# Optimization experiments

Hardware: AMD Instinct MI355X
Metric: run time of the kernel (lower is better)

## Reference

```python
import jax, jax.numpy as jnp
import numpy as np

DIM = 4096
N_HEADS = 32
HEAD_DIM = DIM // N_HEADS  # 128
SEQ = 2048
BATCH = 2


def _rope_freqs(seq_len, head_dim, theta=10000.0):
    inv = 1.0 / (theta ** (np.arange(0, head_dim, 2, dtype=np.float32) / head_dim))
    ang = np.outer(np.arange(seq_len, dtype=np.float32), inv)  # [S, hd/2]
    return jnp.asarray(np.cos(ang)), jnp.asarray(np.sin(ang))


def setup_inputs() -> dict:
    key = jax.random.key(0)
    ks = jax.random.split(key, 10)
    s = 1.0 / np.sqrt(DIM)
    inp = {
        "x": jax.random.normal(ks[0], (BATCH, SEQ, DIM), dtype=jnp.float32),
        "wq_w": jax.random.normal(ks[1], (DIM, DIM), dtype=jnp.float32) * s,
        "wq_b": jax.random.normal(ks[2], (DIM,), dtype=jnp.float32) * 0.01,
        "wk_w": jax.random.normal(ks[3], (DIM, DIM), dtype=jnp.float32) * s,
        "wk_b": jax.random.normal(ks[4], (DIM,), dtype=jnp.float32) * 0.01,
        "wv_w": jax.random.normal(ks[5], (DIM, DIM), dtype=jnp.float32) * s,
        "wv_b": jax.random.normal(ks[6], (DIM,), dtype=jnp.float32) * 0.01,
        "wo_w": jax.random.normal(ks[7], (DIM, DIM), dtype=jnp.float32) * s,
        "wo_b": jax.random.normal(ks[8], (DIM,), dtype=jnp.float32) * 0.01,
    }
    cos, sin = _rope_freqs(SEQ, HEAD_DIM)
    inp["freqs_cos"] = cos  # [S, hd/2]
    inp["freqs_sin"] = sin
    return inp


def _apply_rope(x, cos, sin):
    # x: [B, S, H, D]; cos/sin: [S, D/2] -> broadcast [1, S, 1, D/2]
    B, S, H, D = x.shape
    xr = x.reshape(B, S, H, D // 2, 2)
    re, im = xr[..., 0], xr[..., 1]
    c = cos[None, :, None, :]
    s = sin[None, :, None, :]
    out_re = re * c - im * s
    out_im = re * s + im * c
    return jnp.stack([out_re, out_im], axis=-1).reshape(B, S, H, D)


def reference(x, freqs_cos, freqs_sin, wq_w, wq_b, wk_w, wk_b, wv_w, wv_b, wo_w, wo_b):
    B, S, C = x.shape
    H, D = N_HEADS, HEAD_DIM
    xq = (x @ wq_w.T + wq_b).reshape(B, S, H, D)
    xk = (x @ wk_w.T + wk_b).reshape(B, S, H, D)
    xv = (x @ wv_w.T + wv_b).reshape(B, S, H, D)
    xq = _apply_rope(xq, freqs_cos, freqs_sin)
    xk = _apply_rope(xk, freqs_cos, freqs_sin)
    # [B, H, S, D]
    xq = xq.transpose(0, 2, 1, 3)
    xk = xk.transpose(0, 2, 1, 3)
    xv = xv.transpose(0, 2, 1, 3)
    scale = 1.0 / jnp.sqrt(jnp.asarray(D, dtype=x.dtype))
    scores = jnp.einsum('bhsd,bhtd->bhst', xq, xk) * scale
    causal = jnp.tril(jnp.ones((S, S), dtype=bool))
    scores = jnp.where(causal[None, None], scores, jnp.asarray(-jnp.inf, dtype=scores.dtype))
    attn = jax.nn.softmax(scores, axis=-1)
    y = jnp.einsum('bhst,bhtd->bhsd', attn, xv)  # [B, H, S, D]
    # faithful to source: transpose(-1,-2) then view(B, S, -1) -> raw reshape of [B,H,D,S]
    y = y.transpose(0, 1, 3, 2).reshape(B, S, H * D)
    return y @ wo_w.T + wo_b
```

## Files before the change

### kernel.cpp

```cpp
#include <hip/hip_runtime.h>
#include <hip/hip_bf16.h>

typedef __hip_bfloat16 bf16;
typedef short s16x8 __attribute__((ext_vector_type(8)));
typedef float fx4 __attribute__((ext_vector_type(4)));
typedef unsigned int u32;

#define DIM 4096
#define SEQ 2048
#define NH 32
#define HD 128

#define MFMA_BF16(a,b,c) __builtin_amdgcn_mfma_f32_16x16x32_bf16((a),(b),(c),0,0,0)

__device__ __forceinline__ void gload16(const bf16* g, const bf16* l) {
  __builtin_amdgcn_global_load_lds((const __attribute__((address_space(1))) u32*)g,
                                   (__attribute__((address_space(3))) u32*)l, 16, 0, 0);
}

__global__ void cvt_f32_bf16(const float* __restrict__ in, bf16* __restrict__ out, int n8)
{
  int i = blockIdx.x * blockDim.x + threadIdx.x;
  const int stride = gridDim.x * blockDim.x;
  for (; i < n8; i += stride) {
    fx4 a = ((const fx4*)in)[2 * i], b = ((const fx4*)in)[2 * i + 1];
    s16x8 o; bf16* op = (bf16*)&o;
    #pragma unroll
    for (int j = 0; j < 4; ++j) { op[j] = __float2bfloat16(a[j]); op[4 + j] = __float2bfloat16(b[j]); }
    ((s16x8*)out)[i] = o;
  }
}

__global__ __launch_bounds__(512, 1)
void gemm256(const bf16* __restrict__ A, const bf16* __restrict__ W,
             const float* __restrict__ bias,
             const float* __restrict__ fcos, const float* __restrict__ fsin,
             void* __restrict__ outv, int mode)
{
  __shared__ __align__(16) bf16 As[2][256 * 64];
  __shared__ __align__(16) bf16 Bs[2][256 * 64];
  const int tid = threadIdx.x;
  const int wid = tid >> 6;
  const int lane = tid & 63;
  const int l15 = lane & 15, lg = lane >> 4;
  const int wm = wid >> 2, wn = wid & 3;
  const int brow = blockIdx.y * 256, bcol = blockIdx.x * 256;
  const int rsub = lane >> 3;
  const int scol = ((lane & 7) ^ rsub) * 8;

  fx4 acc[8][4] = {};

  #pragma unroll
  for (int tt = 0; tt < 2; ++tt) {
    #pragma unroll
    for (int j = 0; j < 4; ++j) {
      const int chunk = j * 8 + wid;
      const int row = chunk * 8 + rsub;
      gload16(A + (size_t)(brow + row) * DIM + tt * 64 + scol, &As[tt][chunk * 512]);
      gload16(W + (size_t)(bcol + row) * DIM + tt * 64 + scol, &Bs[tt][chunk * 512]);
    }
  }

  for (int t = 0; t < 64; ++t) {
    const int p = t & 1;
    if (t < 63) asm volatile("s_waitcnt vmcnt(8)" ::: "memory");
    else        asm volatile("s_waitcnt vmcnt(0)" ::: "memory");
    __builtin_amdgcn_s_barrier();
    __builtin_amdgcn_sched_barrier(0);

    s16x8 afr[2][8], bfr[2][4];
    #pragma unroll
    for (int kk = 0; kk < 2; ++kk) {
      #pragma unroll
      for (int mi = 0; mi < 8; ++mi) {
        const int r = wm * 128 + mi * 16 + l15;
        afr[kk][mi] = *(const s16x8*)&As[p][r * 64 + ((((kk * 4 + lg)) ^ (r & 7)) << 3)];
      }
      #pragma unroll
      for (int nj = 0; nj < 4; ++nj) {
        const int r = wn * 64 + nj * 16 + l15;
        bfr[kk][nj] = *(const s16x8*)&Bs[p][r * 64 + ((((kk * 4 + lg)) ^ (r & 7)) << 3)];
      }
    }
    asm volatile("s_waitcnt lgkmcnt(0)" ::: "memory");
    __builtin_amdgcn_sched_barrier(0);
    __builtin_amdgcn_s_barrier();
    __builtin_amdgcn_sched_barrier(0);

    if (t + 2 < 64) {
      const int k0 = (t + 2) * 64;
      #pragma unroll
      for (int j = 0; j < 4; ++j) {
        const int chunk = j * 8 + wid;
        const int row = chunk * 8 + rsub;
        gload16(A + (size_t)(brow + row) * DIM + k0 + scol, &As[p][chunk * 512]);
        gload16(W + (size_t)(bcol + row) * DIM + k0 + scol, &Bs[p][chunk * 512]);
      }
    }

    __builtin_amdgcn_s_setprio(1);
    #pragma unroll
    for (int kk = 0; kk < 2; ++kk)
      #pragma unroll
      for (int mi = 0; mi < 8; ++mi)
        #pragma unroll
        for (int nj = 0; nj < 4; ++nj)
          acc[mi][nj] = MFMA_BF16(afr[kk][mi], bfr[kk][nj], acc[mi][nj]);
    __builtin_amdgcn_s_setprio(0);
  }

  #pragma unroll
  for (int mi = 0; mi < 8; ++mi) {
    const int mbase = brow + wm * 128 + mi * 16 + lg * 4;
    #pragma unroll
    for (int nj = 0; nj < 4; ++nj) {
      const int n = bcol + wn * 64 + nj * 16 + l15;
      const float bv = bias[n];
      #pragma unroll
      for (int r = 0; r < 4; ++r) {
        const int m = mbase + r;
        float val = acc[mi][nj][r] + bv;
        if (mode <= 1) {
          const float pv = __shfl_xor(val, 1);
          const int sp = m & (SEQ - 1);
          const int fi = (n >> 1) & 63;
          const float c = fcos[sp * 64 + fi];
          const float s = fsin[sp * 64 + fi];
          val = (n & 1) ? (pv * s + val * c) : (val * c - pv * s);
        }
        if (mode == 3) {
          ((float*)outv)[(size_t)m * DIM + n] = val;
        } else {
          const int b = m >> 11, sp = m & (SEQ - 1);
          const int h = n >> 7, d = n & (HD - 1);
          ((bf16*)outv)[((size_t)(b * NH + h) * SEQ + sp) * HD + d] = __float2bfloat16(val);
        }
      }
    }
  }
}

__global__ __launch_bounds__(256, 2)
void gemm_slow(const void* __restrict__ Av, const float* __restrict__ Wf,
               const float* __restrict__ bias,
               const float* __restrict__ fcos, const float* __restrict__ fsin,
               void* __restrict__ outv, int mode)
{
  __shared__ __align__(16) bf16 As[128 * 64];
  __shared__ __align__(16) bf16 Bs[128 * 64];
  const int abf = (mode == 3) ? 1 : 0;
  const int tid = threadIdx.x;
  const int wid = tid >> 6;
  const int lane = tid & 63;
  const int l15 = lane & 15, lg = lane >> 4;
  const int wr = wid >> 1, wc = wid & 1;
  const int brow = blockIdx.y * 128, bcol = blockIdx.x * 128;

  fx4 acc[4][4] = {};

  for (int k0 = 0; k0 < DIM; k0 += 64) {
    #pragma unroll
    for (int i = 0; i < 4; ++i) {
      const int v = i * 256 + tid;
      const int row = v >> 3;
      const int c8 = (v & 7) * 8;
      s16x8 a, b;
      if (abf) {
        a = *(const s16x8*)&((const bf16*)Av)[(size_t)(brow + row) * DIM + k0 + c8];
      } else {
        const float* Af = (const float*)Av;
        fx4 a0 = *(const fx4*)&Af[(size_t)(brow + row) * DIM + k0 + c8];
        fx4 a1 = *(const fx4*)&Af[(size_t)(brow + row) * DIM + k0 + c8 + 4];
        bf16* ap = (bf16*)&a;
        #pragma unroll
        for (int j = 0; j < 4; ++j) { ap[j] = __float2bfloat16(a0[j]); ap[4 + j] = __float2bfloat16(a1[j]); }
      }
      {
        fx4 b0 = *(const fx4*)&Wf[(size_t)(bcol + row) * DIM + k0 + c8];
        fx4 b1 = *(const fx4*)&Wf[(size_t)(bcol + row) * DIM + k0 + c8 + 4];
        bf16* bp = (bf16*)&b;
        #pragma unroll
        for (int j = 0; j < 4; ++j) { bp[j] = __float2bfloat16(b0[j]); bp[4 + j] = __float2bfloat16(b1[j]); }
      }
      *(s16x8*)&As[row * 64 + c8] = a;
      *(s16x8*)&Bs[row * 64 + c8] = b;
    }
    __syncthreads();
    #pragma unroll
    for (int kk = 0; kk < 2; ++kk) {
      s16x8 af[4], bfr[4];
      #pragma unroll
      for (int mi = 0; mi < 4; ++mi)
        af[mi] = *(const s16x8*)&As[(wr * 64 + mi * 16 + l15) * 64 + kk * 32 + lg * 8];
      #pragma unroll
      for (int nj = 0; nj < 4; ++nj)
        bfr[nj] = *(const s16x8*)&Bs[(wc * 64 + nj * 16 + l15) * 64 + kk * 32 + lg * 8];
      #pragma unroll
      for (int mi = 0; mi < 4; ++mi)
        #pragma unroll
        for (int nj = 0; nj < 4; ++nj)
          acc[mi][nj] = MFMA_BF16(af[mi], bfr[nj], acc[mi][nj]);
    }
    __syncthreads();
  }

  #pragma unroll
  for (int mi = 0; mi < 4; ++mi) {
    const int mbase = brow + wr * 64 + mi * 16 + lg * 4;
    #pragma unroll
    for (int nj = 0; nj < 4; ++nj) {
      const int n = bcol + wc * 64 + nj * 16 + l15;
      const float bv = bias[n];
      #pragma unroll
      for (int r = 0; r < 4; ++r) {
        const int m = mbase + r;
        float val = acc[mi][nj][r] + bv;
        if (mode <= 1) {
          const float pv = __shfl_xor(val, 1);
          const int sp = m & (SEQ - 1);
          const int fi = (n >> 1) & 63;
          const float c = fcos[sp * 64 + fi];
          const float s = fsin[sp * 64 + fi];
          val = (n & 1) ? (pv * s + val * c) : (val * c - pv * s);
        }
        if (mode == 3) {
          ((float*)outv)[(size_t)m * DIM + n] = val;
        } else {
          const int b = m >> 11, sp = m & (SEQ - 1);
          const int h = n >> 7, d = n & (HD - 1);
          ((bf16*)outv)[((size_t)(b * NH + h) * SEQ + sp) * HD + d] = __float2bfloat16(val);
        }
      }
    }
  }
}

#define SOFTMAX_PHASE(sa, o, mrun, lrun, q0)                                   \
  {                                                                            \
    _Pragma("unroll")                                                          \
    for (int r = 0; r < 4; ++r) {                                              \
      const int q = (q0) + lg * 4 + r;                                         \
      float mx = -__builtin_inff();                                            \
      _Pragma("unroll")                                                        \
      for (int nj = 0; nj < 4; ++nj) {                                         \
        float v = sa[nj][r] * scale;                                           \
        if (diagM && (t0 + nj * 16 + l15 > q)) v = -__builtin_inff();          \
        sa[nj][r] = v;                                                         \
        mx = fmaxf(mx, v);                                                     \
      }                                                                        \
      _Pragma("unroll")                                                        \
      for (int off = 1; off < 16; off <<= 1) mx = fmaxf(mx, __shfl_xor(mx, off)); \
      const float mnew = fmaxf(mrun[r], mx);                                   \
      const float fsc = __expf(mrun[r] - mnew);                                \
      mrun[r] = mnew;                                                          \
      float rs = 0.f;                                                          \
      _Pragma("unroll")                                                        \
      for (int nj = 0; nj < 4; ++nj) {                                         \
        const float pp = __expf(sa[nj][r] - mnew);                             \
        sa[nj][r] = pp;                                                        \
        rs += pp;                                                              \
      }                                                                        \
      _Pragma("unroll")                                                        \
      for (int off = 1; off < 16; off <<= 1) rs += __shfl_xor(rs, off);        \
      lrun[r] = lrun[r] * fsc + rs;                                            \
      _Pragma("unroll")                                                        \
      for (int dj = 0; dj < 8; ++dj) o[dj][r] *= fsc;                          \
    }                                                                          \
  }

__global__ __launch_bounds__(256, 2)
void attn_fwd(const bf16* __restrict__ Q, const bf16* __restrict__ K,
              const bf16* __restrict__ V, bf16* __restrict__ ymat)
{
  __shared__ __align__(16) bf16 smem[32768];
  bf16* Kl   = smem;
  bf16* Vrow = smem + 8192;
  bf16* Vt   = smem + 16384;
  bf16* PlA  = smem + 24576;
  bf16* PlB  = smem + 28672;
  bf16* Ys   = smem;

  const int tid = threadIdx.x, wid = tid >> 6, lane = tid & 63;
  const int l15 = lane & 15, lg = lane >> 4;
  const int pair = blockIdx.x, bh = blockIdx.y;
  const int qtA = pair, qtB = 31 - pair;
  const int b = bh >> 5, h = bh & 31;
  const bf16* Qb = Q + (size_t)bh * SEQ * HD;
  const bf16* Kb = K + (size_t)bh * SEQ * HD;
  const bf16* Vb = V + (size_t)bh * SEQ * HD;
  const int q0A = qtA * 64 + wid * 16;
  const int q0B = qtB * 64 + wid * 16;

  s16x8 aqA[4], aqB[4];
  #pragma unroll
  for (int kk = 0; kk < 4; ++kk) {
    aqA[kk] = *(const s16x8*)&Qb[(size_t)(q0A + l15) * HD + kk * 32 + lg * 8];
    aqB[kk] = *(const s16x8*)&Qb[(size_t)(q0B + l15) * HD + kk * 32 + lg * 8];
  }

  fx4 oA[8] = {}, oB[8] = {};
  float mA[4], lA[4], mB[4], lB[4];
  #pragma unroll
  for (int r = 0; r < 4; ++r) {
    mA[r] = -__builtin_inff(); lA[r] = 0.f;
    mB[r] = -__builtin_inff(); lB[r] = 0.f;
  }
  const float scale = 0.08838834764831845f;

  s16x8 kreg[4], vreg[4];
  #pragma unroll
  for (int i = 0; i < 4; ++i) {
    const int chunk = i * 4 + wid;
    const int row = chunk * 4 + lg;
    const int col = ((l15 ^ (row & 7)) * 8);
    kreg[i] = *(const s16x8*)&Kb[(size_t)row * HD + col];
    vreg[i] = *(const s16x8*)&Vb[(size_t)row * HD + col];
  }

  for (int kt = 0; kt <= qtB; ++kt) {
    const int t0 = kt * 64;
    const bool doA = (kt <= qtA);

    #pragma unroll
    for (int i = 0; i < 4; ++i) {
      const int chunk = i * 4 + wid;
      *(s16x8*)((char*)Kl + chunk * 1024 + lane * 16) = kreg[i];
      *(s16x8*)((char*)Vrow + chunk * 1024 + lane * 16) = vreg[i];
    }
    __syncthreads();

    if (kt < qtB) {
      const int t1 = t0 + 64;
      #pragma unroll
      for (int i = 0; i < 4; ++i) {
        const int chunk = i * 4 + wid;
        const int row = chunk * 4 + lg;
        const int col = ((l15 ^ (row & 7)) * 8);
        kreg[i] = *(const s16x8*)&Kb[(size_t)(t1 + row) * HD + col];
        vreg[i] = *(const s16x8*)&Vb[(size_t)(t1 + row) * HD + col];
      }
    }

    fx4 sA[4], sB[4];
    #pragma unroll
    for (int nj = 0; nj < 4; ++nj) {
      fx4 sa = {}, sb = {};
      #pragma unroll
      for (int kk = 0; kk < 4; ++kk) {
        const int trow = nj * 16 + l15;
        const int colp = (kk * 32 + lg * 8) ^ ((trow & 7) << 3);
        s16x8 bk = *(const s16x8*)&Kl[trow * HD + colp];
        sb = MFMA_BF16(aqB[kk], bk, sb);
        if (doA) sa = MFMA_BF16(aqA[kk], bk, sa);
      }
      sB[nj] = sb; sA[nj] = sa;
    }

    #pragma unroll
    for (int it = 0; it < 2; ++it) {
      const int p = lane;
      const int tg = it * 4 + wid;
      s16x8 lo, hi; bf16* lop = (bf16*)&lo; bf16* hip = (bf16*)&hi;
      #pragma unroll
      for (int j = 0; j < 8; ++j) {
        const int t = tg * 8 + j;
        const u32 v32 = *(const u32*)((const char*)Vrow + t * 256 + ((p * 4) ^ (j << 4)));
        lop[j] = ((const bf16*)&v32)[0];
        hip[j] = ((const bf16*)&v32)[1];
      }
      *(s16x8*)((char*)Vt + (2 * p) * 128 + ((tg * 16) ^ ((p & 7) << 4))) = lo;
      *(s16x8*)((char*)Vt + (2 * p + 1) * 128 + ((tg * 16) ^ ((p & 7) << 4))) = hi;
    }

    {
      const bool diagM = (kt == qtB);
      SOFTMAX_PHASE(sB, oB, mB, lB, q0B)
      #pragma unroll
      for (int r = 0; r < 4; ++r) {
        const int row = lg * 4 + r;
        #pragma unroll
        for (int nj = 0; nj < 4; ++nj) {
          const int colp = (nj * 16 + l15) ^ ((row & 7) << 3);
          PlB[wid * 1024 + row * 64 + colp] = __float2bfloat16(sB[nj][r]);
        }
      }
    }
    if (doA) {
      const bool diagM = (kt == qtA);
      SOFTMAX_PHASE(sA, oA, mA, lA, q0A)
      #pragma unroll
      for (int r = 0; r < 4; ++r) {
        const int row = lg * 4 + r;
        #pragma unroll
        for (int nj = 0; nj < 4; ++nj) {
          const int colp = (nj * 16 + l15) ^ ((row & 7) << 3);
          PlA[wid * 1024 + row * 64 + colp] = __float2bfloat16(sA[nj][r]);
        }
      }
    }
    __syncthreads();

    s16x8 paA[2], paB[2];
    #pragma unroll
    for (int k2 = 0; k2 < 2; ++k2) {
      const int colp = (k2 * 32 + lg * 8) ^ ((l15 & 7) << 3);
      paB[k2] = *(const s16x8*)&PlB[wid * 1024 + l15 * 64 + colp];
      if (doA) paA[k2] = *(const s16x8*)&PlA[wid * 1024 + l15 * 64 + colp];
    }
    #pragma unroll
    for (int dj = 0; dj < 8; ++dj) {
      const int d = dj * 16 + l15;
      #pragma unroll
      for (int k2 = 0; k2 < 2; ++k2) {
        const int colp = (k2 * 32 + lg * 8) ^ (((d >> 1) & 7) << 3);
        s16x8 bv = *(const s16x8*)&Vt[d * 64 + colp];
        oB[dj] = MFMA_BF16(paB[k2], bv, oB[dj]);
        if (doA) oA[dj] = MFMA_BF16(paA[k2], bv, oA[dj]);
      }
    }
    __syncthreads();
  }

  #pragma unroll
  for (int dj = 0; dj < 8; ++dj) {
    const int d = dj * 16 + l15;
    const int lr = d >> 1;
    const int cbase = (d & 1) * 128 + wid * 16 + lg * 4;
    const int sw = (lr & 7) << 3;
    #pragma unroll
    for (int r = 0; r < 4; ++r) {
      Ys[lr * 256 + ((cbase + r) ^ sw)]       = __float2bfloat16(oA[dj][r] / lA[r]);
      Ys[lr * 256 + ((cbase + 64 + r) ^ sw)]  = __float2bfloat16(oB[dj][r] / lB[r]);
    }
  }
  __syncthreads();

  const size_t growbase = (size_t)(b * SEQ + h * 64) * DIM;
  #pragma unroll
  for (int it = 0; it < 8; ++it) {
    const int f = it * 256 + tid;
    const int lr = f >> 5;
    const int cu = f & 31;
    s16x8 v = *(const s16x8*)&Ys[lr * 256 + ((cu ^ (lr & 7)) << 3)];
    const int seg = cu >> 3;
    const int off = (cu & 7) * 8;
    const int par = seg >> 1, ab = seg & 1;
    const int qbase = (ab ? qtB : qtA) * 64;
    *(s16x8*)&ymat[growbase + (size_t)lr * DIM + par * 2048 + qbase + off] = v;
  }
}

extern "C" void kernel_launch(void* const* d_in, const int* in_sizes, int n_in,
                              void* d_out, int out_size, void* d_ws, size_t ws_size,
                              hipStream_t stream)
{
  (void)in_sizes; (void)n_in; (void)out_size;
  const float* x  = (const float*)d_in[0];
  const float* wq = (const float*)d_in[1];
  const float* bq = (const float*)d_in[2];
  const float* wk = (const float*)d_in[3];
  const float* bk = (const float*)d_in[4];
  const float* wv = (const float*)d_in[5];
  const float* bv = (const float*)d_in[6];
  const float* wo = (const float*)d_in[7];
  const float* bo = (const float*)d_in[8];
  const float* fc = (const float*)d_in[9];
  const float* fs = (const float*)d_in[10];

  const size_t NE = (size_t)2 * SEQ * DIM;
  const size_t NW = (size_t)DIM * DIM;
  const size_t SLOT = NE * sizeof(bf16);
  const size_t NEED_FAST = 6 * SLOT + 256;
  const size_t NEED_SLOW = 4 * SLOT + 256;

  dim3 blk(256);
  if (ws_size >= NEED_FAST) {
    bf16* xb = (bf16*)((char*)d_ws + 256);
    bf16* wb = xb + NE;
    bf16* qb = wb + NW;
    bf16* kb = qb + NE;
    bf16* vb = kb + NE;
    bf16* ym = vb + NE;
    const int n8x = (int)(NE / 8), n8w = (int)(NW / 8);
    dim3 cg(2048);
    dim3 blk2(512), gg2(16, 16);
    hipLaunchKernelGGL(cvt_f32_bf16, cg, blk, 0, stream, x, xb, n8x);
    hipLaunchKernelGGL(cvt_f32_bf16, cg, blk, 0, stream, wq, wb, n8w);
    hipLaunchKernelGGL(gemm256, gg2, blk2, 0, stream, xb, wb, bq, fc, fs, qb, 0);
    hipLaunchKernelGGL(cvt_f32_bf16, cg, blk, 0, stream, wk, wb, n8w);
    hipLaunchKernelGGL(gemm256, gg2, blk2, 0, stream, xb, wb, bk, fc, fs, kb, 1);
    hipLaunchKernelGGL(cvt_f32_bf16, cg, blk, 0, stream, wv, wb, n8w);
    hipLaunchKernelGGL(gemm256, gg2, blk2, 0, stream, xb, wb, bv, fc, fs, vb, 2);
    hipLaunchKernelGGL(attn_fwd, dim3(16, 64), blk, 0, stream, qb, kb, vb, ym);
    hipLaunchKernelGGL(cvt_f32_bf16, cg, blk, 0, stream, wo, wb, n8w);
    hipLaunchKernelGGL(gemm256, gg2, blk2, 0, stream, ym, wb, bo, fc, fs, d_out, 3);
  } else if (ws_size >= NEED_SLOW) {
    bf16* qb = (bf16*)((char*)d_ws + 256);
    bf16* kb = qb + NE;
    bf16* vb = kb + NE;
    bf16* ym = vb + NE;
    dim3 gg(32, 32);
    hipLaunchKernelGGL(gemm_slow, gg, blk, 0, stream, x, wq, bq, fc, fs, qb, 0);
    hipLaunchKernelGGL(gemm_slow, gg, blk, 0, stream, x, wk, bk, fc, fs, kb, 1);
    hipLaunchKernelGGL(gemm_slow, gg, blk, 0, stream, x, wv, bv, fc, fs, vb, 2);
    hipLaunchKernelGGL(attn_fwd, dim3(16, 64), blk, 0, stream, qb, kb, vb, ym);
    hipLaunchKernelGGL(gemm_slow, gg, blk, 0, stream, ym, wo, bo, fc, fs, d_out, 3);
  }
}
```

Baseline: 867.6 us.

## Interleave LDS fragment loads with MFMA in four sub-steps per K tile

The GEMM main loop now splits each 64-wide K tile into four quarter-steps. Each quarter loads only a few A/B fragments from LDS and then issues its MFMAs, with s_barrier and setprio placed around each MFMA group. The aim is to overlap LDS reads with matrix math and to cut register pressure by holding 12 fragment registers instead of 24. In exchange it adds several workgroup barriers per iteration, which can add sync stalls, and it relies on the compiler keeping the ordering between waitcnt and the loads.

```diff
diff --git a/kernel.cpp b/kernel.cpp
--- a/kernel.cpp
+++ b/kernel.cpp
@@ -68,25 +68,72 @@
     __builtin_amdgcn_s_barrier();
     __builtin_amdgcn_sched_barrier(0);
 
-    s16x8 afr[2][8], bfr[2][4];
-    #pragma unroll
-    for (int kk = 0; kk < 2; ++kk) {
-      #pragma unroll
-      for (int mi = 0; mi < 8; ++mi) {
-        const int r = wm * 128 + mi * 16 + l15;
-        afr[kk][mi] = *(const s16x8*)&As[p][r * 64 + ((((kk * 4 + lg)) ^ (r & 7)) << 3)];
-      }
-      #pragma unroll
-      for (int nj = 0; nj < 4; ++nj) {
-        const int r = wn * 64 + nj * 16 + l15;
-        bfr[kk][nj] = *(const s16x8*)&Bs[p][r * 64 + ((((kk * 4 + lg)) ^ (r & 7)) << 3)];
-      }
+    s16x8 a0[4], a1[4], b0[4];
+
+    #pragma unroll
+    for (int i = 0; i < 4; ++i) {
+      const int r = wm * 128 + i * 16 + l15;
+      a0[i] = *(const s16x8*)&As[p][r * 64 + (((lg) ^ (r & 7)) << 3)];
+    }
+    #pragma unroll
+    for (int nj = 0; nj < 4; ++nj) {
+      const int r = wn * 64 + nj * 16 + l15;
+      b0[nj] = *(const s16x8*)&Bs[p][r * 64 + (((lg) ^ (r & 7)) << 3)];
+    }
+    __builtin_amdgcn_s_barrier();
+    __builtin_amdgcn_s_setprio(1);
+    #pragma unroll
+    for (int i = 0; i < 4; ++i)
+      #pragma unroll
+      for (int nj = 0; nj < 4; ++nj)
+        acc[i][nj] = MFMA_BF16(a0[i], b0[nj], acc[i][nj]);
+    __builtin_amdgcn_s_setprio(0);
+    __builtin_amdgcn_s_barrier();
+
+    #pragma unroll
+    for (int i = 0; i < 4; ++i) {
+      const int r = wm * 128 + (4 + i) * 16 + l15;
+      a1[i] = *(const s16x8*)&As[p][r * 64 + (((lg) ^ (r & 7)) << 3)];
+    }
+    __builtin_amdgcn_s_barrier();
+    __builtin_amdgcn_s_setprio(1);
+    #pragma unroll
+    for (int i = 0; i < 4; ++i)
+      #pragma unroll
+      for (int nj = 0; nj < 4; ++nj)
+        acc[4 + i][nj] = MFMA_BF16(a1[i], b0[nj], acc[4 + i][nj]);
+    __builtin_amdgcn_s_setprio(0);
+    __builtin_amdgcn_s_barrier();
+
+    #pragma unroll
+    for (int i = 0; i < 4; ++i) {
+      const int r = wm * 128 + i * 16 + l15;
+      a0[i] = *(const s16x8*)&As[p][r * 64 + (((4 + lg) ^ (r & 7)) << 3)];
+    }
+    #pragma unroll
+    for (int nj = 0; nj < 4; ++nj) {
+      const int r = wn * 64 + nj * 16 + l15;
+      b0[nj] = *(const s16x8*)&Bs[p][r * 64 + (((4 + lg) ^ (r & 7)) << 3)];
+    }
+    __builtin_amdgcn_s_barrier();
+    __builtin_amdgcn_s_setprio(1);
+    #pragma unroll
+    for (int i = 0; i < 4; ++i)
+      #pragma unroll
+      for (int nj = 0; nj < 4; ++nj)
+        acc[i][nj] = MFMA_BF16(a0[i], b0[nj], acc[i][nj]);
+    __builtin_amdgcn_s_setprio(0);
+    __builtin_amdgcn_s_barrier();
+
+    #pragma unroll
+    for (int i = 0; i < 4; ++i) {
+      const int r = wm * 128 + (4 + i) * 16 + l15;
+      a1[i] = *(const s16x8*)&As[p][r * 64 + (((4 + lg) ^ (r & 7)) << 3)];
     }
     asm volatile("s_waitcnt lgkmcnt(0)" ::: "memory");
     __builtin_amdgcn_sched_barrier(0);
     __builtin_amdgcn_s_barrier();
     __builtin_amdgcn_sched_barrier(0);
-
     if (t + 2 < 64) {
       const int k0 = (t + 2) * 64;
       #pragma unroll
@@ -97,15 +144,12 @@
         gload16(W + (size_t)(bcol + row) * DIM + k0 + scol, &Bs[p][chunk * 512]);
       }
     }
-
     __builtin_amdgcn_s_setprio(1);
     #pragma unroll
-    for (int kk = 0; kk < 2; ++kk)
-      #pragma unroll
-      for (int mi = 0; mi < 8; ++mi)
-        #pragma unroll
-        for (int nj = 0; nj < 4; ++nj)
-          acc[mi][nj] = MFMA_BF16(afr[kk][mi], bfr[kk][nj], acc[mi][nj]);
+    for (int i = 0; i < 4; ++i)
+      #pragma unroll
+      for (int nj = 0; nj < 4; ++nj)
+        acc[4 + i][nj] = MFMA_BF16(a1[i], b0[nj], acc[4 + i][nj]);
     __builtin_amdgcn_s_setprio(0);
   }
 
```

Result: slower. 905.8 us (+4.4%).

## Fuse Q/K/V projections into one 768-block GEMM launch

Applied to the files above, without the earlier changes.

Merges the three separate QKV projection GEMM launches into a single kernel whose grid covers all three weight matrices, selecting weights, bias and output per block. The K and V bf16 weights are staged in the output buffer as scratch so that all three conversions can happen before the fused launch. The intent is to fill the GPU better, since 256 blocks per launch underfill the 256 CUs with tail effects, and to remove two launch boundaries. Reusing d_out as scratch is safe only because the final GEMM overwrites it later.

```diff
diff --git a/kernel.cpp b/kernel.cpp
--- a/kernel.cpp
+++ b/kernel.cpp
@@ -31,20 +31,18 @@
   }
 }
 
-__global__ __launch_bounds__(512, 1)
-void gemm256(const bf16* __restrict__ A, const bf16* __restrict__ W,
-             const float* __restrict__ bias,
-             const float* __restrict__ fcos, const float* __restrict__ fsin,
-             void* __restrict__ outv, int mode)
-{
-  __shared__ __align__(16) bf16 As[2][256 * 64];
-  __shared__ __align__(16) bf16 Bs[2][256 * 64];
+__device__ __forceinline__
+void gemm256_body(const bf16* __restrict__ A, const bf16* __restrict__ W,
+                  const float* __restrict__ bias,
+                  const float* __restrict__ fcos, const float* __restrict__ fsin,
+                  void* __restrict__ outv, int mode, int brow, int bcol,
+                  bf16 (*As)[256 * 64], bf16 (*Bs)[256 * 64])
+{
   const int tid = threadIdx.x;
   const int wid = tid >> 6;
   const int lane = tid & 63;
   const int l15 = lane & 15, lg = lane >> 4;
   const int wm = wid >> 2, wn = wid & 3;
-  const int brow = blockIdx.y * 256, bcol = blockIdx.x * 256;
   const int rsub = lane >> 3;
   const int scol = ((lane & 7) ^ rsub) * 8;
 
@@ -138,6 +136,35 @@
       }
     }
   }
+}
+
+__global__ __launch_bounds__(512, 1)
+void gemm256(const bf16* __restrict__ A, const bf16* __restrict__ W,
+             const float* __restrict__ bias,
+             const float* __restrict__ fcos, const float* __restrict__ fsin,
+             void* __restrict__ outv, int mode)
+{
+  __shared__ __align__(16) bf16 As[2][256 * 64];
+  __shared__ __align__(16) bf16 Bs[2][256 * 64];
+  gemm256_body(A, W, bias, fcos, fsin, outv, mode,
+               blockIdx.y * 256, blockIdx.x * 256, As, Bs);
+}
+
+__global__ __launch_bounds__(512, 1)
+void gemm_qkv(const bf16* __restrict__ A,
+              const bf16* __restrict__ w0, const bf16* __restrict__ w1, const bf16* __restrict__ w2,
+              const float* __restrict__ b0, const float* __restrict__ b1, const float* __restrict__ b2,
+              const float* __restrict__ fcos, const float* __restrict__ fsin,
+              bf16* __restrict__ o0, bf16* __restrict__ o1, bf16* __restrict__ o2)
+{
+  __shared__ __align__(16) bf16 As[2][256 * 64];
+  __shared__ __align__(16) bf16 Bs[2][256 * 64];
+  const int sel = blockIdx.x >> 4;
+  const bf16* W = (sel == 0) ? w0 : ((sel == 1) ? w1 : w2);
+  const float* bias = (sel == 0) ? b0 : ((sel == 1) ? b1 : b2);
+  void* out = (sel == 0) ? (void*)o0 : ((sel == 1) ? (void*)o1 : (void*)o2);
+  gemm256_body(A, W, bias, fcos, fsin, out, sel,
+               blockIdx.y * 256, (blockIdx.x & 15) * 256, As, Bs);
 }
 
 __global__ __launch_bounds__(256, 2)
@@ -481,19 +508,20 @@
     bf16* kb = qb + NE;
     bf16* vb = kb + NE;
     bf16* ym = vb + NE;
+    bf16* wkb = (bf16*)d_out;
+    bf16* wvb = wkb + NW;
     const int n8x = (int)(NE / 8), n8w = (int)(NW / 8);
     dim3 cg(2048);
-    dim3 blk2(512), gg2(16, 16);
+    dim3 blk2(512);
     hipLaunchKernelGGL(cvt_f32_bf16, cg, blk, 0, stream, x, xb, n8x);
     hipLaunchKernelGGL(cvt_f32_bf16, cg, blk, 0, stream, wq, wb, n8w);
-    hipLaunchKernelGGL(gemm256, gg2, blk2, 0, stream, xb, wb, bq, fc, fs, qb, 0);
-    hipLaunchKernelGGL(cvt_f32_bf16, cg, blk, 0, stream, wk, wb, n8w);
-    hipLaunchKernelGGL(gemm256, gg2, blk2, 0, stream, xb, wb, bk, fc, fs, kb, 1);
-    hipLaunchKernelGGL(cvt_f32_bf16, cg, blk, 0, stream, wv, wb, n8w);
-    hipLaunchKernelGGL(gemm256, gg2, blk2, 0, stream, xb, wb, bv, fc, fs, vb, 2);
+    hipLaunchKernelGGL(cvt_f32_bf16, cg, blk, 0, stream, wk, wkb, n8w);
+    hipLaunchKernelGGL(cvt_f32_bf16, cg, blk, 0, stream, wv, wvb, n8w);
+    hipLaunchKernelGGL(gemm_qkv, dim3(48, 16), blk2, 0, stream,
+                       xb, wb, wkb, wvb, bq, bk, bv, fc, fs, qb, kb, vb);
+    hipLaunchKernelGGL(cvt_f32_bf16, cg, blk, 0, stream, wo, wb, n8w);
     hipLaunchKernelGGL(attn_fwd, dim3(16, 64), blk, 0, stream, qb, kb, vb, ym);
-    hipLaunchKernelGGL(cvt_f32_bf16, cg, blk, 0, stream, wo, wb, n8w);
-    hipLaunchKernelGGL(gemm256, gg2, blk2, 0, stream, ym, wb, bo, fc, fs, d_out, 3);
+    hipLaunchKernelGGL(gemm256, dim3(16, 16), blk2, 0, stream, ym, wb, bo, fc, fs, d_out, 3);
   } else if (ws_size >= NEED_SLOW) {
     bf16* qb = (bf16*)((char*)d_ws + 256);
     bf16* kb = qb + NE;
```

After: 958.2 us. 10.4% more time.
